# Kernel optimization log

Measured on AMD Instinct MI355X. Metric: run time of the kernel, lower is better.

## Reference

```python
import jax, jax.numpy as jnp
from jax import lax
import numpy as np
import math

B, L = 256, 20000
HEADS, HEAD_DIM = 5, 30
W_POOL = (L - 10) // 5 + 1  # 3999, feature dim entering attention
ALPHA = 0.2  # tf.nn.leaky_relu default


def setup_inputs() -> dict:
    key = jax.random.key(0)
    ks = jax.random.split(key, 16)
    n = lambda k, shape: jax.random.normal(k, shape, dtype=jnp.float32) * 0.05
    return {
        "tokens": jax.random.randint(ks[0], (B, L), 0, 4, dtype=jnp.int32),
        "conv1_w": n(ks[1], (4, 10, 1, 5)),   # HWIO
        "conv1_b": jnp.zeros((5,), jnp.float32),
        "conv2_w": n(ks[2], (4, 10, 5, 1)),
        "conv2_b": jnp.zeros((1,), jnp.float32),
        "Wq": n(ks[3], (HEADS, W_POOL, HEAD_DIM)),
        "Wk": n(ks[4], (HEADS, W_POOL, HEAD_DIM)),
        "Wv": n(ks[5], (HEADS, W_POOL, HEAD_DIM)),
        "Wo": n(ks[6], (HEADS * HEAD_DIM, HEAD_DIM)),
        "d1_w": n(ks[7], (4 * HEAD_DIM, 10)),
        "d1_b": jnp.zeros((10,), jnp.float32),
        "d2_w": n(ks[8], (10, 10)),
        "d2_b": jnp.zeros((10,), jnp.float32),
        "d3_w": n(ks[9], (10, 1)),
        "d3_b": jnp.zeros((1,), jnp.float32),
    }


def _forward(tokens, conv1_w, conv1_b, conv2_w, conv2_b,
             Wq, Wk, Wv, Wo, d1_w, d1_b, d2_w, d2_b, d3_w, d3_b):
    dn = ("NHWC", "HWIO", "NHWC")
    # one_hot along axis 1: [B,4,L] -> NHWC image [B,4,L,1]
    x = jax.nn.one_hot(tokens, 4, axis=1, dtype=jnp.float32)[..., None]
    x = lax.conv_general_dilated(x, conv1_w, (1, 1), "SAME", dimension_numbers=dn) + conv1_b
    x = lax.conv_general_dilated(x, conv2_w, (1, 1), "SAME", dimension_numbers=dn) + conv2_b
    # MaxPool2D pool=(1,10), stride=(1,5), VALID -> [B,4,W_POOL,1]
    x = lax.reduce_window(x, -jnp.inf, lax.max, (1, 1, 10, 1), (1, 1, 5, 1), "VALID")
    x = x.reshape(x.shape[0], 4, -1)  # [B, S=4, D=W_POOL]
    S = x.shape[1]
    # batched multi-head causal self-attention (fused over heads)
    q = jnp.einsum("bsd,hde->bhse", x, Wq)
    k = jnp.einsum("bsd,hde->bhse", x, Wk)
    v = jnp.einsum("bsd,hde->bhse", x, Wv)
    scores = jnp.einsum("bhse,bhte->bhst", q, k) / math.sqrt(HEAD_DIM)
    mask = jnp.triu(jnp.full((S, S), -jnp.inf, dtype=jnp.float32), k=1)
    attn = jax.nn.softmax(scores + mask, axis=-1)
    o = jnp.einsum("bhst,bhte->bshe", attn, v).reshape(x.shape[0], S, HEADS * HEAD_DIM)
    o = o @ Wo  # [B, 4, 30]
    h = o.reshape(o.shape[0], -1)  # flatten -> [B, 120]
    h = jax.nn.leaky_relu(h @ d1_w + d1_b, ALPHA)
    h = jax.nn.leaky_relu(h @ d2_w + d2_b, ALPHA)
    return jax.nn.sigmoid(h @ d3_w + d3_b)  # [B, 1]


def reference(tokens, conv1_w, conv1_b, conv2_w, conv2_b,
              Wq, Wk, Wv, Wo, d1_w, d1_b, d2_w, d2_b, d3_w, d3_b):
    return _forward(tokens, conv1_w, conv1_b, conv2_w, conv2_b,
                    Wq, Wk, Wv, Wo, d1_w, d1_b, d2_w, d2_b, d3_w, d3_b)
```

## Files before the change

### kernel.cpp

```cpp
#include <hip/hip_runtime.h>
#include <math.h>

#define Bb 256
#define Ll 20000
#define WPOOL 3999
#define HEADS 5
#define HDIM 30
#define NB_K1 (Bb*16)
#define WBBLK 960
#define PADABLK 388
#define PS2 (Bb*1800)

#define WS_F    0
#define WS_BIAS 368
#define WS_G    384
#define WS_FBL  1288
#define WS_FBR  2728
#define WS_BBL  4528
#define WS_BBR  4544
#define WS_X    4608
#define WS_P    (WS_X + Bb*WPOOL*4)
#define WS_A    (WS_P + 4*PS2)
#define WS_WB   (WS_A + 1024*4096/2)

typedef short short8 __attribute__((ext_vector_type(8)));
typedef float f32x4 __attribute__((ext_vector_type(4)));

__device__ __forceinline__ unsigned short f2bf(float f) {
    unsigned u = __float_as_uint(f);
    return (unsigned short)((u + 0x7FFFu + ((u >> 16) & 1u)) >> 16);
}

__device__ __forceinline__ float tbl_entry(const float* __restrict__ WP,
    int t, int d, int i, int kw2min, int kw2max)
{
    if (t >= 4) return 0.f;
    float p[4] = {0.f, 0.f, 0.f, 0.f};
#pragma unroll
    for (int kh = 0; kh < 4; ++kh) {
        int r = i + kh - 1;
        if (r < 0 || r > 3) continue;
        int kh1 = t - r + 1;
        if (kh1 < 0 || kh1 > 3) continue;
        int lo = d - kw2max; if (lo < 0) lo = 0;
        int hi = d - kw2min; if (hi > 9) hi = 9;
        const float* wpa = WP + (kh1 * 10) * 40 + kh * 10;
        for (int kw1 = lo; kw1 <= hi; ++kw1)
            p[kh] += wpa[kw1 * 40 + (d - kw1)];
    }
    return (p[0] + p[1]) + (p[2] + p[3]);
}

__global__ __launch_bounds__(256) void k0_build(const float* __restrict__ w1g,
    const float* __restrict__ b1g, const float* __restrict__ w2g,
    const float* __restrict__ b2g,
    const float* __restrict__ Wq, const float* __restrict__ Wk,
    const float* __restrict__ Wv, float* __restrict__ ws)
{
    const int tid = threadIdx.x;

    if (blockIdx.x >= 14) {
        int xb = blockIdx.x - 14;
        unsigned short* Au = reinterpret_cast<unsigned short*>(ws + WS_A);
        unsigned short* WBu = reinterpret_cast<unsigned short*>(ws + WS_WB);
        if (xb < WBBLK) {
            int idx = xb * 256 + tid;
            int n = idx >> 9;
            int k0 = (idx & 511) * 8;
            unsigned short vals[8];
            if (n < 450) {
                int proj = n / 150, hh = (n % 150) / 30, e = n % 30;
                const float* Wm = (proj == 0) ? Wq : ((proj == 1) ? Wk : Wv);
                const float* base = Wm + (size_t)hh * WPOOL * 30 + e;
#pragma unroll
                for (int j = 0; j < 8; ++j) {
                    int k = k0 + j;
                    vals[j] = (k < WPOOL) ? f2bf(base[(size_t)k * 30]) : (unsigned short)0;
                }
            } else {
#pragma unroll
                for (int j = 0; j < 8; ++j) vals[j] = 0;
            }
            unsigned v0 = (unsigned)vals[0] | ((unsigned)vals[1] << 16);
            unsigned v1 = (unsigned)vals[2] | ((unsigned)vals[3] << 16);
            unsigned v2 = (unsigned)vals[4] | ((unsigned)vals[5] << 16);
            unsigned v3 = (unsigned)vals[6] | ((unsigned)vals[7] << 16);
            *reinterpret_cast<uint4*>(WBu + (size_t)n * 4096 + k0) =
                make_uint4(v0, v1, v2, v3);
        } else {
            int idx = (xb - WBBLK) * 256 + tid;
            if (idx < 1024 * 97) {
                int row = idx / 97;
                int kk = WPOOL + idx % 97;
                Au[(size_t)row * 4096 + kk] = 0;
            }
        }
        return;
    }

    __shared__ float w1[200], w2[200], b1[5], WP[1600], SB[40], Fsh[360];
    __shared__ float b2v;

    for (int i = tid; i < 200; i += 256) {
        w1[i] = w1g[i];
        w2[i] = w2g[i];
    }
    if (tid < 5) b1[tid] = b1g[tid];
    if (tid == 5) b2v = b2g[0];
    __syncthreads();

    for (int idx = tid; idx < 1600; idx += 256) {
        int a = idx / 40, b = idx % 40;
        float acc = 0.f;
#pragma unroll
        for (int c = 0; c < 5; ++c) acc += w1[a * 5 + c] * w2[b * 5 + c];
        WP[idx] = acc;
    }
    if (tid < 40) {
        float acc = 0.f;
#pragma unroll
        for (int c = 0; c < 5; ++c) acc += b1[c] * w2[tid * 5 + c];
        SB[tid] = acc;
    }
    __syncthreads();

    if (blockIdx.x == 0) {
        for (int idx = tid; idx < 360; idx += 256) {
            int t = idx / 72, d = (idx / 4) % 18, i = idx % 4;
            float v = tbl_entry(WP, t, d, i, 0, 9);
            Fsh[idx] = v;
            ws[WS_F + idx] = v;
        }
        if (tid < 4) {
            int i = tid;
            float acc = b2v;
#pragma unroll
            for (int kh = 0; kh < 4; ++kh) {
                int r = i + kh - 1;
                if (r < 0 || r > 3) continue;
                for (int kw2 = 0; kw2 < 10; ++kw2) acc += SB[kh * 10 + kw2];
            }
            ws[WS_BIAS + i] = acc;
        }
        __syncthreads();
        for (int idx = tid; idx < 900; idx += 256) {
            int p = idx / 36, j = (idx / 4) % 9, i = idx % 4;
            int t0 = p / 5, t1 = p % 5;
            ws[WS_G + idx] = Fsh[(t0 * 18 + 2 * j) * 4 + i]
                           + Fsh[(t1 * 18 + 2 * j + 1) * 4 + i];
        }
    } else {
        int gidx = (blockIdx.x - 1) * 256 + tid;
        if (gidx < 3240) {
            int wslot = gidx / 360, rem = gidx % 360;
            int t = rem / 72, d = (rem / 4) % 18, i = rem % 4;
            bool left = wslot < 4;
            int wloc = left ? wslot : wslot - 4;
            int kw2min = left ? 4 - wloc : 0;
            int kw2max = left ? 9 : 8 - wloc;
            float v = tbl_entry(WP, t, d, i, kw2min, kw2max);
            ws[(left ? WS_FBL + wloc * 360 : WS_FBR + wloc * 360) + rem] = v;
        } else if (gidx < 3276) {
            int bs = gidx - 3240;
            int wslot = bs / 4, i = bs % 4;
            bool left = wslot < 4;
            int wloc = left ? wslot : wslot - 4;
            int kw2min = left ? 4 - wloc : 0;
            int kw2max = left ? 9 : 8 - wloc;
            float acc = b2v;
#pragma unroll
            for (int kh = 0; kh < 4; ++kh) {
                int r = i + kh - 1;
                if (r < 0 || r > 3) continue;
                for (int kw2 = kw2min; kw2 <= kw2max; ++kw2)
                    acc += SB[kh * 10 + kw2];
            }
            ws[(left ? WS_BBL + wloc * 4 : WS_BBR + wloc * 4) + i] = acc;
        }
    }
}

__global__ __launch_bounds__(256) void k1_convpool(const int* __restrict__ tokens,
    const float* __restrict__ ws_c, float* __restrict__ ws)
{
    __shared__ int tok[1280];
    __shared__ float4 Gs[225];
    __shared__ float4 m5[256];
    __shared__ float4 biasS;

    const int tid = threadIdx.x;
    const int b = blockIdx.x >> 4;
    const int chunk = blockIdx.x & 15;
    const int p0 = chunk * 250;
    const int pcnt = min(250, WPOOL - p0);
    const int colBase = 5 * p0 - 8;

    const float4* Gg = reinterpret_cast<const float4*>(ws_c + WS_G);
    for (int j = tid; j < 225; j += 256) Gs[j] = Gg[j];
    if (tid == 0) biasS = *reinterpret_cast<const float4*>(ws_c + WS_BIAS);
    const int* tb = tokens + (size_t)b * Ll;
    for (int j = tid; j < 1280; j += 256) {
        int u = colBase + j;
        tok[j] = (u >= 0 && u < Ll) ? tb[u] : 4;
    }
    __syncthreads();

    if (tid <= pcnt) {
        const int W = 5 * (p0 + tid);
        int tk[22];
#pragma unroll
        for (int m = 0; m < 22; ++m) tk[m] = tok[5 * tid + m];

        float4 mymax;
        const bool isLeft = (chunk == 0 && tid == 0);
        const bool isRight = (W + 4 >= Ll - 5);
        if (!isLeft && !isRight) {
            float4 bias4 = biasS;
            bool first = true;
#pragma unroll
            for (int c = 0; c < 5; ++c) {
                float a0 = bias4.x, a1 = bias4.y, a2 = bias4.z, a3 = bias4.w;
#pragma unroll
                for (int j = 0; j < 9; ++j) {
                    int pc = tk[c + 2 * j] * 5 + tk[c + 2 * j + 1];
                    float4 g = Gs[pc * 9 + j];
                    a0 += g.x; a1 += g.y; a2 += g.z; a3 += g.w;
                }
                if (first) { mymax = make_float4(a0, a1, a2, a3); first = false; }
                else {
                    mymax.x = fmaxf(mymax.x, a0); mymax.y = fmaxf(mymax.y, a1);
                    mymax.z = fmaxf(mymax.z, a2); mymax.w = fmaxf(mymax.w, a3);
                }
            }
        } else {
            bool first = true;
            for (int c = 0; c < 5; ++c) {
                int w = W + c;
                const float* T; const float* Bv;
                if (w < 4)            { T = ws_c + WS_FBL + w * 360;           Bv = ws_c + WS_BBL + 4 * w; }
                else if (w >= Ll - 5) { T = ws_c + WS_FBR + (w - (Ll - 5)) * 360; Bv = ws_c + WS_BBR + 4 * (w - (Ll - 5)); }
                else                  { T = ws_c + WS_F;                        Bv = ws_c + WS_BIAS; }
                float a0 = Bv[0], a1 = Bv[1], a2 = Bv[2], a3 = Bv[3];
                for (int d = 0; d < 18; ++d) {
                    const float* f = T + (size_t)(tk[c + d] * 18 + d) * 4;
                    a0 += f[0]; a1 += f[1]; a2 += f[2]; a3 += f[3];
                }
                if (first) { mymax = make_float4(a0, a1, a2, a3); first = false; }
                else {
                    mymax.x = fmaxf(mymax.x, a0); mymax.y = fmaxf(mymax.y, a1);
                    mymax.z = fmaxf(mymax.z, a2); mymax.w = fmaxf(mymax.w, a3);
                }
            }
        }
        m5[tid] = mymax;
    }
    __syncthreads();

    if (tid < pcnt) {
        float4 a = m5[tid], c = m5[tid + 1];
        a.x = fmaxf(a.x, c.x); a.y = fmaxf(a.y, c.y);
        a.z = fmaxf(a.z, c.z); a.w = fmaxf(a.w, c.w);
        const int k = p0 + tid;
        unsigned short* Au = reinterpret_cast<unsigned short*>(ws + WS_A);
        Au[(size_t)(b * 4 + 0) * 4096 + k] = f2bf(a.x);
        Au[(size_t)(b * 4 + 1) * 4096 + k] = f2bf(a.y);
        Au[(size_t)(b * 4 + 2) * 4096 + k] = f2bf(a.z);
        Au[(size_t)(b * 4 + 3) * 4096 + k] = f2bf(a.w);
    }
}

__global__ __launch_bounds__(256) void k2_mfma(const unsigned short* __restrict__ A,
    const unsigned short* __restrict__ WB, float* __restrict__ P0,
    float* __restrict__ P1)
{
    const int wave = threadIdx.x >> 6;
    const int lane = threadIdx.x & 63;
    const int mg = blockIdx.x & 15;
    const int rest = blockIdx.x >> 4;
    const int ng = rest % 6;
    const int ks = rest / 6;
    const int m0 = (mg * 4 + wave) * 16;
    const int n0 = ng * 80;
    const int kbase = ks * 512;

    const int lrow = lane & 15;
    const int lk = (lane >> 4) * 8;

    const unsigned short* Ap = A + (size_t)(m0 + lrow) * 4096 + kbase + lk;
    const unsigned short* Bp = WB + (size_t)(n0 + lrow) * 4096 + kbase + lk;

    f32x4 acc0 = {0.f, 0.f, 0.f, 0.f};
    f32x4 acc1 = acc0, acc2 = acc0, acc3 = acc0, acc4 = acc0;

#pragma unroll 4
    for (int step = 0; step < 16; ++step) {
        const unsigned short* ap = Ap + step * 32;
        const unsigned short* bp = Bp + step * 32;
        short8 af = *reinterpret_cast<const short8*>(ap);
        short8 b0 = *reinterpret_cast<const short8*>(bp);
        short8 b1 = *reinterpret_cast<const short8*>(bp + (size_t)16 * 4096);
        short8 b2 = *reinterpret_cast<const short8*>(bp + (size_t)32 * 4096);
        short8 b3 = *reinterpret_cast<const short8*>(bp + (size_t)48 * 4096);
        short8 b4 = *reinterpret_cast<const short8*>(bp + (size_t)64 * 4096);
        acc0 = __builtin_amdgcn_mfma_f32_16x16x32_bf16(af, b0, acc0, 0, 0, 0);
        acc1 = __builtin_amdgcn_mfma_f32_16x16x32_bf16(af, b1, acc1, 0, 0, 0);
        acc2 = __builtin_amdgcn_mfma_f32_16x16x32_bf16(af, b2, acc2, 0, 0, 0);
        acc3 = __builtin_amdgcn_mfma_f32_16x16x32_bf16(af, b3, acc3, 0, 0, 0);
        acc4 = __builtin_amdgcn_mfma_f32_16x16x32_bf16(af, b4, acc4, 0, 0, 0);
    }

    const int rbase = (lane >> 4) * 4;
    float* Pb = (ks < 4) ? (P0 + (size_t)ks * PS2) : (P1 + (size_t)(ks - 4) * PS2);
#define STORE(ACC, T) do {                                              \
        int col = n0 + (T) * 16 + lrow;                                 \
        if (col < 450) {                                                \
            _Pragma("unroll")                                           \
            for (int r = 0; r < 4; ++r) {                               \
                int m = m0 + rbase + r;                                 \
                Pb[(size_t)(m >> 2) * 1800 + (m & 3) * 450 + col] = ACC[r]; \
            }                                                           \
        }                                                               \
    } while (0)
    STORE(acc0, 0); STORE(acc1, 1); STORE(acc2, 2); STORE(acc3, 3); STORE(acc4, 4);
#undef STORE
}

__global__ __launch_bounds__(256) void k3_attn(const float* __restrict__ Wo,
    const float* __restrict__ d1w, const float* __restrict__ d1b,
    const float* __restrict__ d2w, const float* __restrict__ d2b,
    const float* __restrict__ d3w, const float* __restrict__ d3b,
    const float* __restrict__ ws, float* __restrict__ out)
{
    __shared__ float Qs[5][4][30], Ks2[5][4][30], Vs[5][4][30];
    __shared__ float sc[5][4][4];
    __shared__ float ob[4][150];
    __shared__ float hb[120], h1[10], h2[10];
    const int tid = threadIdx.x;
    const int b = blockIdx.x;
    const float* P0 = ws + WS_P + (size_t)b * 1800;
    const float* P1 = ws + WS_X + (size_t)b * 1800;

    for (int idx = tid; idx < 1800; idx += 256) {
        float val = 0.f;
#pragma unroll
        for (int ks = 0; ks < 4; ++ks)
            val += P0[(size_t)ks * PS2 + idx] + P1[(size_t)ks * PS2 + idx];
        int s = idx / 450, n = idx % 450;
        int proj = n / 150, hh = (n % 150) / 30, e = n % 30;
        if (proj == 0)      Qs[hh][s][e] = val;
        else if (proj == 1) Ks2[hh][s][e] = val;
        else                Vs[hh][s][e] = val;
    }
    __syncthreads();

    if (tid < 80) {
        int hh = tid >> 4, s = (tid >> 2) & 3, t = tid & 3;
        float a = 0.f;
        if (t <= s) {
            for (int e = 0; e < 30; ++e) a += Qs[hh][s][e] * Ks2[hh][t][e];
            a *= (1.0f / sqrtf(30.0f));
        }
        sc[hh][s][t] = a;
    }
    __syncthreads();

    if (tid < 20) {
        int hh = tid / 4, s = tid % 4;
        float m = -1e30f;
        for (int t = 0; t <= s; ++t) m = fmaxf(m, sc[hh][s][t]);
        float ex[4]; float den = 0.f;
        for (int t = 0; t <= s; ++t) { ex[t] = expf(sc[hh][s][t] - m); den += ex[t]; }
        for (int t = 0; t < 4; ++t) sc[hh][s][t] = (t <= s) ? ex[t] / den : 0.f;
    }
    __syncthreads();

    for (int idx = tid; idx < 600; idx += 256) {
        int s = idx / 150, j = idx % 150, hh = j / 30, e = j % 30;
        float a = 0.f;
        for (int t = 0; t < 4; ++t) a += sc[hh][s][t] * Vs[hh][t][e];
        ob[s][j] = a;
    }
    __syncthreads();

    if (tid < 120) {
        int s = tid / 30, e2 = tid % 30;
        float a = 0.f;
        for (int j = 0; j < 150; ++j) a += ob[s][j] * Wo[j * 30 + e2];
        hb[s * 30 + e2] = a;
    }
    __syncthreads();

    if (tid < 10) {
        float a = d1b[tid];
        for (int i = 0; i < 120; ++i) a += hb[i] * d1w[i * 10 + tid];
        h1[tid] = a > 0.f ? a : 0.2f * a;
    }
    __syncthreads();
    if (tid < 10) {
        float a = d2b[tid];
        for (int i = 0; i < 10; ++i) a += h1[i] * d2w[i * 10 + tid];
        h2[tid] = a > 0.f ? a : 0.2f * a;
    }
    __syncthreads();
    if (tid == 0) {
        float a = d3b[0];
        for (int i = 0; i < 10; ++i) a += h2[i] * d3w[i];
        out[b] = 1.f / (1.f + expf(-a));
    }
}

extern "C" void kernel_launch(void* const* d_in, const int* in_sizes, int n_in,
                              void* d_out, int out_size, void* d_ws, size_t ws_size,
                              hipStream_t stream)
{
    const int*   tokens = (const int*)d_in[0];
    const float* c1w = (const float*)d_in[1];
    const float* c1b = (const float*)d_in[2];
    const float* c2w = (const float*)d_in[3];
    const float* c2b = (const float*)d_in[4];
    const float* Wq  = (const float*)d_in[5];
    const float* Wk  = (const float*)d_in[6];
    const float* Wv  = (const float*)d_in[7];
    const float* Wo  = (const float*)d_in[8];
    const float* d1w = (const float*)d_in[9];
    const float* d1b = (const float*)d_in[10];
    const float* d2w = (const float*)d_in[11];
    const float* d2b = (const float*)d_in[12];
    const float* d3w = (const float*)d_in[13];
    const float* d3b = (const float*)d_in[14];
    float* ws = (float*)d_ws;
    float* out = (float*)d_out;

    k0_build<<<14 + WBBLK + PADABLK, 256, 0, stream>>>(c1w, c1b, c2w, c2b,
                                                       Wq, Wk, Wv, ws);
    k1_convpool<<<NB_K1, 256, 0, stream>>>(tokens, ws, ws);
    k2_mfma<<<16 * 6 * 8, 256, 0, stream>>>(
        reinterpret_cast<const unsigned short*>(ws + WS_A),
        reinterpret_cast<const unsigned short*>(ws + WS_WB),
        ws + WS_P, ws + WS_X);
    k3_attn<<<Bb, 256, 0, stream>>>(Wo, d1w, d1b, d2w, d2b, d3w, d3b, ws, out);
}
```

Measured before the change: 89.16 us.

## Coalesce weight bf16 transpose via LDS tiles and use 3-token lookup tables

The weight transpose/convert in k0 now stages contiguous tiles of Wq/Wk/Wv in shared memory, so global reads are coalesced instead of strided by 30. Zero padding for the unused rows gets its own blocks. The conv+pool kernel replaces the 2-token pair table with a 3-token triple table, so each output needs 6 LDS lookups instead of 9, in exchange for a larger shared table (750 float4). The workspace layout is also reshuffled, dropping the old X region and renaming the partial buffers.

Measured after the change: 96.52 us. 1.08x slower.

```diff
diff --git a/kernel.cpp b/kernel.cpp
--- a/kernel.cpp
+++ b/kernel.cpp
@@ -7,20 +7,21 @@
 #define HEADS 5
 #define HDIM 30
 #define NB_K1 (Bb*16)
-#define WBBLK 960
+#define WBCBLK 240
+#define WBPADBLK 2
 #define PADABLK 388
 #define PS2 (Bb*1800)
 
 #define WS_F    0
 #define WS_BIAS 368
-#define WS_G    384
-#define WS_FBL  1288
-#define WS_FBR  2728
-#define WS_BBL  4528
-#define WS_BBR  4544
-#define WS_X    4608
-#define WS_P    (WS_X + Bb*WPOOL*4)
-#define WS_A    (WS_P + 4*PS2)
+#define WS_FBL  384
+#define WS_FBR  1824
+#define WS_BBL  3624
+#define WS_BBR  3640
+#define WS_G3   3664
+#define WS_P0   8192
+#define WS_P1   (WS_P0 + 4*PS2)
+#define WS_A    (WS_P1 + 4*PS2)
 #define WS_WB   (WS_A + 1024*4096/2)
 
 typedef short short8 __attribute__((ext_vector_type(8)));
@@ -63,32 +64,46 @@
         int xb = blockIdx.x - 14;
         unsigned short* Au = reinterpret_cast<unsigned short*>(ws + WS_A);
         unsigned short* WBu = reinterpret_cast<unsigned short*>(ws + WS_WB);
-        if (xb < WBBLK) {
-            int idx = xb * 256 + tid;
-            int n = idx >> 9;
-            int k0 = (idx & 511) * 8;
-            unsigned short vals[8];
-            if (n < 450) {
-                int proj = n / 150, hh = (n % 150) / 30, e = n % 30;
-                const float* Wm = (proj == 0) ? Wq : ((proj == 1) ? Wk : Wv);
-                const float* base = Wm + (size_t)hh * WPOOL * 30 + e;
-#pragma unroll
-                for (int j = 0; j < 8; ++j) {
-                    int k = k0 + j;
-                    vals[j] = (k < WPOOL) ? f2bf(base[(size_t)k * 30]) : (unsigned short)0;
+        if (xb < WBCBLK) {
+            __shared__ float wtile[7680];
+            const int ph = xb >> 4;
+            const int k0 = (xb & 15) * 256;
+            const int hh = ph % 5, proj = ph / 5;
+            const float* Wm = (proj == 0) ? Wq : ((proj == 1) ? Wk : Wv);
+            const float* base = Wm + (size_t)hh * WPOOL * 30;
+            const int lim = WPOOL * 30;
+            for (int j = tid; j < 7680; j += 256) {
+                int gi = k0 * 30 + j;
+                wtile[j] = (gi < lim) ? base[gi] : 0.f;
+            }
+            __syncthreads();
+#pragma unroll
+            for (int pass = 0; pass < 4; ++pass) {
+                int e = pass * 8 + (tid >> 5);
+                if (e < 30) {
+                    int kk0 = (tid & 31) * 8;
+                    unsigned short vals[8];
+#pragma unroll
+                    for (int j = 0; j < 8; ++j)
+                        vals[j] = f2bf(wtile[(kk0 + j) * 30 + e]);
+                    unsigned v0 = (unsigned)vals[0] | ((unsigned)vals[1] << 16);
+                    unsigned v1 = (unsigned)vals[2] | ((unsigned)vals[3] << 16);
+                    unsigned v2 = (unsigned)vals[4] | ((unsigned)vals[5] << 16);
+                    unsigned v3 = (unsigned)vals[6] | ((unsigned)vals[7] << 16);
+                    *reinterpret_cast<uint4*>(
+                        WBu + (size_t)(ph * 30 + e) * 4096 + k0 + kk0) =
+                        make_uint4(v0, v1, v2, v3);
                 }
-            } else {
-#pragma unroll
-                for (int j = 0; j < 8; ++j) vals[j] = 0;
-            }
-            unsigned v0 = (unsigned)vals[0] | ((unsigned)vals[1] << 16);
-            unsigned v1 = (unsigned)vals[2] | ((unsigned)vals[3] << 16);
-            unsigned v2 = (unsigned)vals[4] | ((unsigned)vals[5] << 16);
-            unsigned v3 = (unsigned)vals[6] | ((unsigned)vals[7] << 16);
-            *reinterpret_cast<uint4*>(WBu + (size_t)n * 4096 + k0) =
-                make_uint4(v0, v1, v2, v3);
+            }
+        } else if (xb < WBCBLK + WBPADBLK) {
+            int s0 = (xb - WBCBLK) * 256 + tid;
+            for (int s = s0; s < 30 * 512; s += WBPADBLK * 256) {
+                int row = 450 + s / 512, koff = (s % 512) * 8;
+                *reinterpret_cast<uint4*>(WBu + (size_t)row * 4096 + koff) =
+                    make_uint4(0, 0, 0, 0);
+            }
         } else {
-            int idx = (xb - WBBLK) * 256 + tid;
+            int idx = (xb - WBCBLK - WBPADBLK) * 256 + tid;
             if (idx < 1024 * 97) {
                 int row = idx / 97;
                 int kk = WPOOL + idx % 97;
@@ -143,11 +158,12 @@
             ws[WS_BIAS + i] = acc;
         }
         __syncthreads();
-        for (int idx = tid; idx < 900; idx += 256) {
-            int p = idx / 36, j = (idx / 4) % 9, i = idx % 4;
-            int t0 = p / 5, t1 = p % 5;
-            ws[WS_G + idx] = Fsh[(t0 * 18 + 2 * j) * 4 + i]
-                           + Fsh[(t1 * 18 + 2 * j + 1) * 4 + i];
+        for (int idx = tid; idx < 3000; idx += 256) {
+            int combo = idx / 24, g = (idx / 4) % 6, i = idx % 4;
+            int t0 = combo / 25, t1 = (combo / 5) % 5, t2 = combo % 5;
+            ws[WS_G3 + idx] = Fsh[(t0 * 18 + 3 * g) * 4 + i]
+                            + Fsh[(t1 * 18 + 3 * g + 1) * 4 + i]
+                            + Fsh[(t2 * 18 + 3 * g + 2) * 4 + i];
         }
     } else {
         int gidx = (blockIdx.x - 1) * 256 + tid;
@@ -184,7 +200,7 @@
     const float* __restrict__ ws_c, float* __restrict__ ws)
 {
     __shared__ int tok[1280];
-    __shared__ float4 Gs[225];
+    __shared__ float4 G3s[750];
     __shared__ float4 m5[256];
     __shared__ float4 biasS;
 
@@ -195,8 +211,8 @@
     const int pcnt = min(250, WPOOL - p0);
     const int colBase = 5 * p0 - 8;
 
-    const float4* Gg = reinterpret_cast<const float4*>(ws_c + WS_G);
-    for (int j = tid; j < 225; j += 256) Gs[j] = Gg[j];
+    const float4* Gg = reinterpret_cast<const float4*>(ws_c + WS_G3);
+    for (int j = tid; j < 750; j += 256) G3s[j] = Gg[j];
     if (tid == 0) biasS = *reinterpret_cast<const float4*>(ws_c + WS_BIAS);
     const int* tb = tokens + (size_t)b * Ll;
     for (int j = tid; j < 1280; j += 256) {
@@ -221,10 +237,11 @@
             for (int c = 0; c < 5; ++c) {
                 float a0 = bias4.x, a1 = bias4.y, a2 = bias4.z, a3 = bias4.w;
 #pragma unroll
-                for (int j = 0; j < 9; ++j) {
-                    int pc = tk[c + 2 * j] * 5 + tk[c + 2 * j + 1];
-                    float4 g = Gs[pc * 9 + j];
-                    a0 += g.x; a1 += g.y; a2 += g.z; a3 += g.w;
+                for (int g = 0; g < 6; ++g) {
+                    int pc = tk[c + 3 * g] * 25 + tk[c + 3 * g + 1] * 5
+                           + tk[c + 3 * g + 2];
+                    float4 v = G3s[pc * 6 + g];
+                    a0 += v.x; a1 += v.y; a2 += v.z; a3 += v.w;
                 }
                 if (first) { mymax = make_float4(a0, a1, a2, a3); first = false; }
                 else {
@@ -337,8 +354,8 @@
     __shared__ float hb[120], h1[10], h2[10];
     const int tid = threadIdx.x;
     const int b = blockIdx.x;
-    const float* P0 = ws + WS_P + (size_t)b * 1800;
-    const float* P1 = ws + WS_X + (size_t)b * 1800;
+    const float* P0 = ws + WS_P0 + (size_t)b * 1800;
+    const float* P1 = ws + WS_P1 + (size_t)b * 1800;
 
     for (int idx = tid; idx < 1800; idx += 256) {
         float val = 0.f;
@@ -431,12 +448,12 @@
     float* ws = (float*)d_ws;
     float* out = (float*)d_out;
 
-    k0_build<<<14 + WBBLK + PADABLK, 256, 0, stream>>>(c1w, c1b, c2w, c2b,
-                                                       Wq, Wk, Wv, ws);
+    k0_build<<<14 + WBCBLK + WBPADBLK + PADABLK, 256, 0, stream>>>(
+        c1w, c1b, c2w, c2b, Wq, Wk, Wv, ws);
     k1_convpool<<<NB_K1, 256, 0, stream>>>(tokens, ws, ws);
     k2_mfma<<<16 * 6 * 8, 256, 0, stream>>>(
         reinterpret_cast<const unsigned short*>(ws + WS_A),
         reinterpret_cast<const unsigned short*>(ws + WS_WB),
-        ws + WS_P, ws + WS_X);
+        ws + WS_P0, ws + WS_P1);
     k3_attn<<<Bb, 256, 0, stream>>>(Wo, d1w, d1b, d2w, d2b, d3w, d3b, ws, out);
 }
```
